# Kernel tuning notes

Hardware: AMD Instinct MI355X
Metric: run time of the kernel (lower is better)

Reference implementation:

```python
import jax, jax.numpy as jnp
import numpy as np

B, T, E, H = 4, 1024, 768, 12
DH = E // H
MAXP = 64  # rel_max_positions per relation type
SCALE = DH ** -0.5


def _sinusoid_embed(max_pos, dim):
    # fairseq-style sinusoid table with padding row 0 zeroed
    num = max_pos + 1
    half = dim // 2
    freq = np.exp(np.arange(half) * -(np.log(10000.0) / (half - 1)))
    ang = np.arange(num)[:, None] * freq[None, :]
    emb = np.concatenate([np.sin(ang), np.cos(ang)], axis=1)
    emb[0] = 0.0
    return jnp.asarray(emb, dtype=jnp.float32)


def _xavier(key, out_d, in_d, gain):
    bound = gain * np.sqrt(6.0 / (in_d + out_d))
    return jax.random.uniform(key, (out_d, in_d), jnp.float32, -bound, bound)


def setup_inputs() -> dict:
    key = jax.random.key(0)
    ks = jax.random.split(key, 16)
    g = 1.0 / np.sqrt(2.0)
    inp = {
        'x': jax.random.normal(ks[0], (B, T, E), jnp.float32),
        'rel_pos0': jax.random.randint(ks[1], (T, T), 0, MAXP + 1),
        'rel_pos1': jax.random.randint(ks[2], (T, T), 0, MAXP + 1),
        'rel_emb0': _sinusoid_embed(MAXP, E),
        'rel_emb1': _sinusoid_embed(MAXP, E),
    }
    names = ['Wq_r', 'Wk_r', 'Wv_r', 'Wq_s', 'Wk_s', 'Wv_s', 'Wk2', 'Wv2', 'Wrel0', 'Wrel1']
    for i, n in enumerate(names):
        inp[n] = _xavier(ks[3 + i], E, E, g)
        inp[n.replace('W', 'b', 1)] = jnp.zeros((E,), jnp.float32)
    inp['Wo'] = _xavier(ks[13], E, E, 1.0)
    inp['bo'] = jnp.zeros((E,), jnp.float32)
    return inp


def _lin(x, W, b):
    return x @ W.T + b


def _heads(x):
    return x.reshape(x.shape[0], x.shape[1], H, DH).transpose(0, 2, 1, 3)  # [B,H,T,DH]


def reference(x, rel_pos0, rel_pos1, rel_emb0, rel_emb1,
              Wq_r, bq_r, Wk_r, bk_r, Wv_r, bv_r,
              Wq_s, bq_s, Wk_s, bk_s, Wv_s, bv_s,
              Wk2, bk2, Wv2, bv2,
              Wrel0, brel0, Wrel1, brel1, Wo, bo):
    # --- sum branch: plain attention producing per-position summaries ---
    qs = _heads(_lin(x, Wq_s, bq_s)) * SCALE
    ks_ = _heads(_lin(x, Wk_s, bk_s))
    vs = _heads(_lin(x, Wv_s, bv_s))
    attn_s = jax.nn.softmax(jnp.einsum('bhqd,bhkd->bhqk', qs, ks_), axis=-1)
    sum_x = jnp.einsum('bhqk,bhkd->bhqd', attn_s, vs).transpose(0, 2, 1, 3).reshape(B, T, E)
    # summaries re-projected as extra keys/values for the reg branch
    k2 = _heads(_lin(sum_x, Wk2, bk2))
    v2 = _heads(_lin(sum_x, Wv2, bv2))
    # --- reg branch with per-relation-type RPE score biases ---
    q = _heads(_lin(x, Wq_r, bq_r)) * SCALE
    k = _heads(_lin(x, Wk_r, bk_r))
    v = _heads(_lin(x, Wv_r, bv_r))
    s_reg = jnp.einsum('bhqd,bhkd->bhqk', q, k)
    for rel_pos, rel_emb, Wr, br in ((rel_pos0, rel_emb0, Wrel0, brel0),
                                     (rel_pos1, rel_emb1, Wrel1, brel1)):
        table = _lin(rel_emb, Wr, br).reshape(-1, H, DH)       # [P,H,DH]
        ts = jnp.einsum('bhqd,phd->bhqp', q, table)            # [B,H,T,P]
        idx = jnp.broadcast_to(rel_pos[None, None], (B, H, T, T))
        s_reg = s_reg + jnp.take_along_axis(ts, idx, axis=3)   # RPE gather
    s_sum = jnp.einsum('bhqd,bhkd->bhqk', q, k2)
    attn = jax.nn.softmax(jnp.concatenate([s_reg, s_sum], axis=-1), axis=-1)  # [B,H,T,2T]
    kv = jnp.concatenate([v, v2], axis=2)                       # [B,H,2T,DH]
    out = jnp.einsum('bhqk,bhkd->bhqd', attn, kv).transpose(0, 2, 1, 3).reshape(B, T, E)
    return _lin(out, Wo, bo)
```

## Files before the change

kernel.cpp:

```cpp
#include <hip/hip_runtime.h>
#include <hip/hip_bf16.h>
#include <stdint.h>


#define DEV __device__ __forceinline__

using f32x4 = __attribute__((ext_vector_type(4))) float;
using s16x8 = __attribute__((ext_vector_type(8))) short;
using s16x4 = __attribute__((ext_vector_type(4))) short;
using i32x4 = __attribute__((ext_vector_type(4))) int;
using fvec4 = __attribute__((ext_vector_type(4))) float;
using u16 = unsigned short;

static constexpr int KD = 768;
static constexpr int PE = 4096 * 768;

DEV u16 f2bf(float f) {
  uint32_t u = __builtin_bit_cast(uint32_t, f);
  u += 0x7FFF + ((u >> 16) & 1);
  return (u16)(u >> 16);
}
DEV float bf2f(u16 h) { return __builtin_bit_cast(float, (uint32_t)h << 16); }

DEV void gload16(const void* g, void* l) {
  __builtin_amdgcn_global_load_lds((const __attribute__((address_space(1))) void*)g,
                                   (__attribute__((address_space(3))) void*)l, 16, 0, 0);
}
DEV f32x4 mfma16(s16x8 a, s16x8 b, f32x4 c) {
  return __builtin_amdgcn_mfma_f32_16x16x32_bf16(a, b, c, 0, 0, 0);
}

struct CastJobs {
  const float* src[14];
  u16* dst[14];
  int n[14];
};
__global__ __launch_bounds__(256) void cast_bf16_kernel(CastJobs J) {
  const int job = blockIdx.y;
  const int i = (blockIdx.x * 256 + threadIdx.x) * 8;
  if (i >= J.n[job]) return;
  const fvec4* s = (const fvec4*)(J.src[job] + i);
  fvec4 a = s[0], b = s[1];
  s16x8 o;
  o[0] = (short)f2bf(a[0]); o[1] = (short)f2bf(a[1]);
  o[2] = (short)f2bf(a[2]); o[3] = (short)f2bf(a[3]);
  o[4] = (short)f2bf(b[0]); o[5] = (short)f2bf(b[1]);
  o[6] = (short)f2bf(b[2]); o[7] = (short)f2bf(b[3]);
  *(s16x8*)(J.dst[job] + i) = o;
}

__global__ __launch_bounds__(256) void pack_rp_kernel(const int* rp0, const int* rp1, u16* outp) {
  const int i = (blockIdx.x * 256 + threadIdx.x) * 8;
  i32x4 a0 = *(const i32x4*)(rp0 + i), a1 = *(const i32x4*)(rp0 + i + 4);
  i32x4 b0 = *(const i32x4*)(rp1 + i), b1 = *(const i32x4*)(rp1 + i + 4);
  s16x8 o;
  o[0] = (short)(a0[0] | (b0[0] << 8));
  o[1] = (short)(a0[1] | (b0[1] << 8));
  o[2] = (short)(a0[2] | (b0[2] << 8));
  o[3] = (short)(a0[3] | (b0[3] << 8));
  o[4] = (short)(a1[0] | (b1[0] << 8));
  o[5] = (short)(a1[1] | (b1[1] << 8));
  o[6] = (short)(a1[2] | (b1[2] << 8));
  o[7] = (short)(a1[3] | (b1[3] << 8));
  *(s16x8*)(outp + i) = o;
}

struct GemmP {
  const u16* A;
  const u16* Bw;
  const float* bias[6];
  u16* out_bf;
  float* out_f;
  int epi;
};

__global__ __launch_bounds__(256) void gemm_bt(GemmP p) {
  __shared__ __align__(16) u16 As[128 * 64];
  __shared__ __align__(16) u16 Bs[128 * 64];
  const int tid = threadIdx.x;
  const int m0 = blockIdx.x * 128, n0 = blockIdx.y * 128;
  const u16* Ag = p.A + (size_t)m0 * KD;
  const u16* Bg = p.Bw + (size_t)n0 * KD;
  const int lane = tid & 63, wid = tid >> 6;
  const int wm = (wid >> 1) * 64, wn = (wid & 1) * 64;
  const int lhi = lane >> 4, llo = lane & 15;

  uint ldso[4], srco[4];
#pragma unroll
  for (int j = 0; j < 4; ++j) {
    uint o = tid * 16 + j * 4096;
    uint row = o >> 7, kc = (o >> 4) & 7;
    ldso[j] = o;
    srco[j] = row * KD + ((kc ^ (row & 7)) << 3);
  }

  f32x4 acc[4][4] = {};

  for (int kt = 0; kt < 12; ++kt) {
    const int k0 = kt * 64;
#pragma unroll
    for (int j = 0; j < 4; ++j) gload16(Ag + srco[j] + k0, (char*)As + ldso[j]);
#pragma unroll
    for (int j = 0; j < 4; ++j) gload16(Bg + srco[j] + k0, (char*)Bs + ldso[j]);
    __syncthreads();
#pragma unroll
    for (int kf = 0; kf < 2; ++kf) {
      s16x8 av[4], bv[4];
#pragma unroll
      for (int mf = 0; mf < 4; ++mf) {
        int r = wm + mf * 16 + llo;
        av[mf] = *(const s16x8*)&As[r * 64 + ((((kf << 2) | lhi) ^ (r & 7)) << 3)];
      }
#pragma unroll
      for (int nf = 0; nf < 4; ++nf) {
        int r = wn + nf * 16 + llo;
        bv[nf] = *(const s16x8*)&Bs[r * 64 + ((((kf << 2) | lhi) ^ (r & 7)) << 3)];
      }
#pragma unroll
      for (int mf = 0; mf < 4; ++mf)
#pragma unroll
        for (int nf = 0; nf < 4; ++nf)
          acc[mf][nf] = mfma16(av[mf], bv[nf], acc[mf][nf]);
    }
    __syncthreads();
  }

  const int epi = p.epi;
#pragma unroll
  for (int nf = 0; nf < 4; ++nf) {
    const int n = n0 + wn + nf * 16 + llo;
    int proj = 0, n1 = n, hh, dd;
    float bias, scale = 1.0f;
    if (epi <= 1) {
      proj = n / 768; n1 = n - proj * 768;
      hh = n1 >> 6; dd = n1 & 63;
      bias = p.bias[proj][n1];
      if (epi == 0 && (proj == 0 || proj == 3)) scale = 0.125f;
    } else {
      hh = n >> 6; dd = n & 63;
      bias = p.bias[0][n];
    }
#pragma unroll
    for (int mf = 0; mf < 4; ++mf) {
      f32x4 c = acc[mf][nf];
      const int mb = m0 + wm + mf * 16 + lhi * 4;
      if (epi == 3) {
#pragma unroll
        for (int r = 0; r < 4; ++r)
          p.out_f[(size_t)(mb + r) * 768 + n] = c[r] + bias;
      } else if (epi == 2) {
#pragma unroll
        for (int r = 0; r < 4; ++r) {
          int m = mb + r;
          if (m < 80) p.out_bf[((size_t)hh * 80 + m) * 64 + dd] = f2bf(c[r] + bias);
        }
      } else {
        const bool vlay = (epi == 0) ? (proj == 2 || proj == 5) : (proj == 1);
        if (vlay) {
          const int b = mb >> 10, t = mb & 1023;
          const int bh = b * 12 + hh;
          s16x4 o4;
          o4[0] = (short)f2bf((c[0] + bias) * scale);
          o4[1] = (short)f2bf((c[1] + bias) * scale);
          o4[2] = (short)f2bf((c[2] + bias) * scale);
          o4[3] = (short)f2bf((c[3] + bias) * scale);
          *(s16x4*)&p.out_bf[(size_t)proj * PE + ((size_t)(bh * 64 + dd)) * 1024 + t] = o4;
        } else {
#pragma unroll
          for (int r = 0; r < 4; ++r) {
            int m = mb + r;
            int b = m >> 10, t = m & 1023;
            int bh = b * 12 + hh;
            p.out_bf[(size_t)proj * PE + ((size_t)(bh * 1024 + t)) * 64 + dd] =
                f2bf((c[r] + bias) * scale);
          }
        }
      }
    }
  }
}

__global__ __launch_bounds__(256) void sum_attn_kernel(const u16* Qs, const u16* Ks,
                                                       const u16* Vst, u16* sum_x) {
  __shared__ __align__(16) u16 kbuf[64 * 64];
  __shared__ __align__(16) u16 vbuf[64 * 64];
  __shared__ __align__(16) u16 pbuf[4][16 * 72];
  const int tid = threadIdx.x, lane = tid & 63, w = tid >> 6;
  const int lhi = lane >> 4, llo = lane & 15;
  const int qt = blockIdx.x, bh = blockIdx.y;
  const int qbase = qt * 64 + w * 16;

  const u16* Qg = Qs + ((size_t)bh * 1024 + qbase + llo) * 64;
  s16x8 aq0 = *(const s16x8*)(Qg + lhi * 8);
  s16x8 aq1 = *(const s16x8*)(Qg + 32 + lhi * 8);

  f32x4 accO[4] = {};
  float mrun[4], lrun[4];
#pragma unroll
  for (int r = 0; r < 4; ++r) { mrun[r] = -1e30f; lrun[r] = 0.f; }

  uint so[2], srow[2], sswz[2];
#pragma unroll
  for (int j = 0; j < 2; ++j) {
    uint o = tid * 16 + j * 4096;
    so[j] = o; srow[j] = o >> 7;
    sswz[j] = (((o >> 4) & 7) ^ (srow[j] & 7)) << 3;
  }
  const u16* Kg = Ks + (size_t)bh * 65536;
  const u16* Vg = Vst + (size_t)bh * 65536;

  for (int kt = 0; kt < 16; ++kt) {
#pragma unroll
    for (int j = 0; j < 2; ++j) {
      gload16(Kg + (size_t)kt * 4096 + srow[j] * 64 + sswz[j], (char*)kbuf + so[j]);
      gload16(Vg + (size_t)srow[j] * 1024 + kt * 64 + sswz[j], (char*)vbuf + so[j]);
    }
    __syncthreads();

    f32x4 s[4];
#pragma unroll
    for (int kc4 = 0; kc4 < 4; ++kc4) {
      f32x4 c = {};
#pragma unroll
      for (int kf = 0; kf < 2; ++kf) {
        int kr = kc4 * 16 + llo;
        s16x8 bk = *(const s16x8*)&kbuf[kr * 64 + ((((kf << 2) | lhi) ^ (kr & 7)) << 3)];
        c = mfma16(kf ? aq1 : aq0, bk, c);
      }
      s[kc4] = c;
    }

    float pmax[4], corr[4], lpart[4];
#pragma unroll
    for (int r = 0; r < 4; ++r)
      pmax[r] = fmaxf(fmaxf(s[0][r], s[1][r]), fmaxf(s[2][r], s[3][r]));
#pragma unroll
    for (int msk = 1; msk < 16; msk <<= 1)
#pragma unroll
      for (int r = 0; r < 4; ++r)
        pmax[r] = fmaxf(pmax[r], __shfl_xor(pmax[r], msk, 64));
#pragma unroll
    for (int r = 0; r < 4; ++r) {
      float mn = fmaxf(mrun[r], pmax[r]);
      corr[r] = __expf(mrun[r] - mn);
      mrun[r] = mn; lpart[r] = 0.f;
    }
#pragma unroll
    for (int kc4 = 0; kc4 < 4; ++kc4)
#pragma unroll
      for (int r = 0; r < 4; ++r) {
        float pv = __expf(s[kc4][r] - mrun[r]);
        lpart[r] += pv;
        pbuf[w][(lhi * 4 + r) * 72 + kc4 * 16 + llo] = f2bf(pv);
      }
#pragma unroll
    for (int msk = 1; msk < 16; msk <<= 1)
#pragma unroll
      for (int r = 0; r < 4; ++r)
        lpart[r] += __shfl_xor(lpart[r], msk, 64);
#pragma unroll
    for (int r = 0; r < 4; ++r) lrun[r] = lrun[r] * corr[r] + lpart[r];
#pragma unroll
    for (int dc = 0; dc < 4; ++dc)
#pragma unroll
      for (int r = 0; r < 4; ++r) accO[dc][r] *= corr[r];

    asm volatile("s_waitcnt lgkmcnt(0)" ::: "memory");
    __builtin_amdgcn_sched_barrier(0);

#pragma unroll
    for (int kf = 0; kf < 2; ++kf) {
      s16x8 ap = *(const s16x8*)&pbuf[w][llo * 72 + kf * 32 + lhi * 8];
#pragma unroll
      for (int dc = 0; dc < 4; ++dc) {
        int dr = dc * 16 + llo;
        s16x8 bv = *(const s16x8*)&vbuf[dr * 64 + ((((kf << 2) | lhi) ^ (dr & 7)) << 3)];
        accO[dc] = mfma16(ap, bv, accO[dc]);
      }
    }
    __syncthreads();
  }

  const int b = bh / 12, hh = bh - b * 12;
#pragma unroll
  for (int dc = 0; dc < 4; ++dc)
#pragma unroll
    for (int r = 0; r < 4; ++r) {
      int q = qbase + lhi * 4 + r;
      float o = accO[dc][r] / lrun[r];
      sum_x[((size_t)b * 1024 + q) * 768 + hh * 64 + dc * 16 + llo] = f2bf(o);
    }
}

__global__ __launch_bounds__(256) void reg_attn_kernel(
    const u16* Qr, const u16* Kr, const u16* Vrt,
    const u16* K2, const u16* V2t,
    const u16* tab0, const u16* tab1,
    const u16* rpk, u16* attn_out) {
  __shared__ __align__(16) u16 kbuf[64 * 64];
  __shared__ __align__(16) u16 vbuf[64 * 64];
  __shared__ __align__(16) u16 tsb[2][64 * 80];
  __shared__ __align__(16) u16 pbuf[4][16 * 72];
  const int tid = threadIdx.x, lane = tid & 63, w = tid >> 6;
  const int lhi = lane >> 4, llo = lane & 15;
  const int qt = blockIdx.x, bh = blockIdx.y;
  const int b = bh / 12, hh = bh - b * 12;
  const int qbase = qt * 64 + w * 16;

  const u16* Qg = Qr + ((size_t)bh * 1024 + qbase + llo) * 64;
  s16x8 aq0 = *(const s16x8*)(Qg + lhi * 8);
  s16x8 aq1 = *(const s16x8*)(Qg + 32 + lhi * 8);

#pragma unroll
  for (int tt = 0; tt < 2; ++tt) {
    const u16* tb = tt ? tab1 : tab0;
#pragma unroll
    for (int pf = 0; pf < 5; ++pf) {
      f32x4 c = {};
#pragma unroll
      for (int kf = 0; kf < 2; ++kf) {
        s16x8 bt = *(const s16x8*)(tb + ((size_t)hh * 80 + pf * 16 + llo) * 64 + kf * 32 + lhi * 8);
        c = mfma16(kf ? aq1 : aq0, bt, c);
      }
#pragma unroll
      for (int r = 0; r < 4; ++r)
        tsb[tt][(w * 16 + lhi * 4 + r) * 80 + pf * 16 + llo] = f2bf(c[r]);
    }
  }
  __syncthreads();

  f32x4 accO[4] = {};
  float mrun[4], lrun[4];
#pragma unroll
  for (int r = 0; r < 4; ++r) { mrun[r] = -1e30f; lrun[r] = 0.f; }

  uint so[2], srow[2], sswz[2];
#pragma unroll
  for (int j = 0; j < 2; ++j) {
    uint o = tid * 16 + j * 4096;
    so[j] = o; srow[j] = o >> 7;
    sswz[j] = (((o >> 4) & 7) ^ (srow[j] & 7)) << 3;
  }
  const u16* KgA = Kr + (size_t)bh * 65536;
  const u16* KgB = K2 + (size_t)bh * 65536;
  const u16* VgA = Vrt + (size_t)bh * 65536;
  const u16* VgB = V2t + (size_t)bh * 65536;

  for (int kt = 0; kt < 32; ++kt) {
    const bool ph1 = kt < 16;
    const int kk = ph1 ? kt : kt - 16;
    const u16* Kg = ph1 ? KgA : KgB;
    const u16* Vg = ph1 ? VgA : VgB;
#pragma unroll
    for (int j = 0; j < 2; ++j) {
      gload16(Kg + (size_t)kk * 4096 + srow[j] * 64 + sswz[j], (char*)kbuf + so[j]);
      gload16(Vg + (size_t)srow[j] * 1024 + kk * 64 + sswz[j], (char*)vbuf + so[j]);
    }
    __syncthreads();

    f32x4 s[4];
#pragma unroll
    for (int kc4 = 0; kc4 < 4; ++kc4) {
      f32x4 c = {};
#pragma unroll
      for (int kf = 0; kf < 2; ++kf) {
        int kr = kc4 * 16 + llo;
        s16x8 bk = *(const s16x8*)&kbuf[kr * 64 + ((((kf << 2) | lhi) ^ (kr & 7)) << 3)];
        c = mfma16(kf ? aq1 : aq0, bk, c);
      }
      s[kc4] = c;
    }

    if (ph1) {
      u16 pp[16];
#pragma unroll
      for (int kc4 = 0; kc4 < 4; ++kc4)
#pragma unroll
        for (int r = 0; r < 4; ++r)
          pp[kc4 * 4 + r] =
              rpk[(size_t)(qbase + lhi * 4 + r) * 1024 + kt * 64 + kc4 * 16 + llo];
#pragma unroll
      for (int kc4 = 0; kc4 < 4; ++kc4)
#pragma unroll
        for (int r = 0; r < 4; ++r) {
          u16 v = pp[kc4 * 4 + r];
          int ql = w * 16 + lhi * 4 + r;
          s[kc4][r] += bf2f(tsb[0][ql * 80 + (v & 255)]) + bf2f(tsb[1][ql * 80 + (v >> 8)]);
        }
    }

    float pmax[4], corr[4], lpart[4];
#pragma unroll
    for (int r = 0; r < 4; ++r)
      pmax[r] = fmaxf(fmaxf(s[0][r], s[1][r]), fmaxf(s[2][r], s[3][r]));
#pragma unroll
    for (int msk = 1; msk < 16; msk <<= 1)
#pragma unroll
      for (int r = 0; r < 4; ++r)
        pmax[r] = fmaxf(pmax[r], __shfl_xor(pmax[r], msk, 64));
#pragma unroll
    for (int r = 0; r < 4; ++r) {
      float mn = fmaxf(mrun[r], pmax[r]);
      corr[r] = __expf(mrun[r] - mn);
      mrun[r] = mn; lpart[r] = 0.f;
    }
#pragma unroll
    for (int kc4 = 0; kc4 < 4; ++kc4)
#pragma unroll
      for (int r = 0; r < 4; ++r) {
        float pv = __expf(s[kc4][r] - mrun[r]);
        lpart[r] += pv;
        pbuf[w][(lhi * 4 + r) * 72 + kc4 * 16 + llo] = f2bf(pv);
      }
#pragma unroll
    for (int msk = 1; msk < 16; msk <<= 1)
#pragma unroll
      for (int r = 0; r < 4; ++r)
        lpart[r] += __shfl_xor(lpart[r], msk, 64);
#pragma unroll
    for (int r = 0; r < 4; ++r) lrun[r] = lrun[r] * corr[r] + lpart[r];
#pragma unroll
    for (int dc = 0; dc < 4; ++dc)
#pragma unroll
      for (int r = 0; r < 4; ++r) accO[dc][r] *= corr[r];

    asm volatile("s_waitcnt lgkmcnt(0)" ::: "memory");
    __builtin_amdgcn_sched_barrier(0);

#pragma unroll
    for (int kf = 0; kf < 2; ++kf) {
      s16x8 ap = *(const s16x8*)&pbuf[w][llo * 72 + kf * 32 + lhi * 8];
#pragma unroll
      for (int dc = 0; dc < 4; ++dc) {
        int dr = dc * 16 + llo;
        s16x8 bv = *(const s16x8*)&vbuf[dr * 64 + ((((kf << 2) | lhi) ^ (dr & 7)) << 3)];
        accO[dc] = mfma16(ap, bv, accO[dc]);
      }
    }
    __syncthreads();
  }

#pragma unroll
  for (int dc = 0; dc < 4; ++dc)
#pragma unroll
    for (int r = 0; r < 4; ++r) {
      int q = qbase + lhi * 4 + r;
      float o = accO[dc][r] / lrun[r];
      attn_out[((size_t)b * 1024 + q) * 768 + hh * 64 + dc * 16 + llo] = f2bf(o);
    }
}

extern "C" void kernel_launch(void* const* d_in, const int* in_sizes, int n_in,
                              void* d_out, int out_size, void* d_ws, size_t ws_size,
                              hipStream_t stream) {
  (void)in_sizes; (void)n_in; (void)out_size; (void)ws_size;
  const float* x     = (const float*)d_in[0];
  const int*   rp0   = (const int*)d_in[1];
  const int*   rp1   = (const int*)d_in[2];
  const float* re0   = (const float*)d_in[3];
  const float* re1   = (const float*)d_in[4];
  const float* Wq_r  = (const float*)d_in[5];  const float* bq_r = (const float*)d_in[6];
  const float* Wk_r  = (const float*)d_in[7];  const float* bk_r = (const float*)d_in[8];
  const float* Wv_r  = (const float*)d_in[9];  const float* bv_r = (const float*)d_in[10];
  const float* Wq_s  = (const float*)d_in[11]; const float* bq_s = (const float*)d_in[12];
  const float* Wk_s  = (const float*)d_in[13]; const float* bk_s = (const float*)d_in[14];
  const float* Wv_s  = (const float*)d_in[15]; const float* bv_s = (const float*)d_in[16];
  const float* Wk2   = (const float*)d_in[17]; const float* bk2  = (const float*)d_in[18];
  const float* Wv2   = (const float*)d_in[19]; const float* bv2  = (const float*)d_in[20];
  const float* Wrel0 = (const float*)d_in[21]; const float* brel0 = (const float*)d_in[22];
  const float* Wrel1 = (const float*)d_in[23]; const float* brel1 = (const float*)d_in[24];
  const float* Wo    = (const float*)d_in[25]; const float* bo   = (const float*)d_in[26];
  float* out = (float*)d_out;

  char* wp = (char*)d_ws;
  auto carve = [&](size_t bytes) {
    char* r = wp;
    wp += (bytes + 255) & ~(size_t)255;
    return r;
  };
  u16* xb     = (u16*)carve((size_t)PE * 2);
  u16* Wcat1  = (u16*)carve((size_t)4608 * 768 * 2);
  u16* Wcat2  = (u16*)carve((size_t)1536 * 768 * 2);
  u16* Wrel0b = (u16*)carve((size_t)768 * 768 * 2);
  u16* Wrel1b = (u16*)carve((size_t)768 * 768 * 2);
  u16* Wob    = (u16*)carve((size_t)768 * 768 * 2);
  u16* relA0  = (u16*)carve((size_t)128 * 768 * 2);
  u16* relA1  = (u16*)carve((size_t)128 * 768 * 2);
  u16* qkv    = (u16*)carve((size_t)6 * PE * 2);
  u16* k2v2   = (u16*)carve((size_t)2 * PE * 2);
  u16* tb0    = (u16*)carve((size_t)12 * 80 * 64 * 2);
  u16* tb1    = (u16*)carve((size_t)12 * 80 * 64 * 2);
  u16* rpk    = (u16*)carve((size_t)1024 * 1024 * 2);
  u16* sumx   = (u16*)carve((size_t)PE * 2);
  u16* aout   = (u16*)carve((size_t)PE * 2);

  const int wn_ = 768 * 768;
  CastJobs J;
  const float* srcs[14] = {x, Wq_r, Wk_r, Wv_r, Wq_s, Wk_s, Wv_s, Wk2, Wv2, Wrel0, Wrel1, Wo, re0, re1};
  u16* dsts[14] = {xb, Wcat1, Wcat1 + wn_, Wcat1 + 2 * wn_, Wcat1 + 3 * wn_, Wcat1 + 4 * wn_,
                   Wcat1 + 5 * wn_, Wcat2, Wcat2 + wn_, Wrel0b, Wrel1b, Wob, relA0, relA1};
  int ns[14] = {PE, wn_, wn_, wn_, wn_, wn_, wn_, wn_, wn_, wn_, wn_, wn_, 65 * 768, 65 * 768};
  for (int i = 0; i < 14; ++i) { J.src[i] = srcs[i]; J.dst[i] = dsts[i]; J.n[i] = ns[i]; }
  cast_bf16_kernel<<<dim3(1536, 14), 256, 0, stream>>>(J);

  pack_rp_kernel<<<dim3(512), 256, 0, stream>>>(rp0, rp1, rpk);

  GemmP g1{};
  g1.A = xb; g1.Bw = Wcat1;
  g1.bias[0] = bq_r; g1.bias[1] = bk_r; g1.bias[2] = bv_r;
  g1.bias[3] = bq_s; g1.bias[4] = bk_s; g1.bias[5] = bv_s;
  g1.out_bf = qkv; g1.epi = 0;
  gemm_bt<<<dim3(32, 36), 256, 0, stream>>>(g1);

  GemmP gt0{}; gt0.A = relA0; gt0.Bw = Wrel0b; gt0.bias[0] = brel0; gt0.out_bf = tb0; gt0.epi = 2;
  gemm_bt<<<dim3(1, 6), 256, 0, stream>>>(gt0);
  GemmP gt1{}; gt1.A = relA1; gt1.Bw = Wrel1b; gt1.bias[0] = brel1; gt1.out_bf = tb1; gt1.epi = 2;
  gemm_bt<<<dim3(1, 6), 256, 0, stream>>>(gt1);

  sum_attn_kernel<<<dim3(16, 48), 256, 0, stream>>>(qkv + (size_t)3 * PE, qkv + (size_t)4 * PE,
                                                    qkv + (size_t)5 * PE, sumx);

  GemmP g2{};
  g2.A = sumx; g2.Bw = Wcat2; g2.bias[0] = bk2; g2.bias[1] = bv2;
  g2.out_bf = k2v2; g2.epi = 1;
  gemm_bt<<<dim3(32, 12), 256, 0, stream>>>(g2);

  reg_attn_kernel<<<dim3(16, 48), 256, 0, stream>>>(qkv, qkv + (size_t)PE, qkv + (size_t)2 * PE,
                                                    k2v2, k2v2 + (size_t)PE, tb0, tb1, rpk, aout);

  GemmP gf{};
  gf.A = aout; gf.Bw = Wob; gf.bias[0] = bo; gf.out_f = out; gf.epi = 3;
  gemm_bt<<<dim3(32, 6), 256, 0, stream>>>(gf);
}
```

Before: 434.9 us.

## Lazy softmax rescale, deferred row-sum reduction, XCD-aware block remap in attention kernels

Both attention kernels now skip the cross-lane max reduction and accumulator rescale when no row max grows by more than 8 over the running max (wave-uniform check). Row sums stay as per-lane partials and are reduced once after the loop. Blocks are launched on a 1D grid and remapped so the 8 chunks of 96 consecutive (head, q-tile) work items each land on one XCD, improving L2 reuse of K/V. MFMA sections run under raised wave priority. The reg kernel splits its loop into two specialised phases and issues the RPE index loads before the barrier. The lazy max adds a small risk of bf16 precision loss when exp values reach up to e^8.

```diff
diff --git a/kernel.cpp b/kernel.cpp
--- a/kernel.cpp
+++ b/kernel.cpp
@@ -187,7 +187,9 @@
   __shared__ __align__(16) u16 pbuf[4][16 * 72];
   const int tid = threadIdx.x, lane = tid & 63, w = tid >> 6;
   const int lhi = lane >> 4, llo = lane & 15;
-  const int qt = blockIdx.x, bh = blockIdx.y;
+  const int bid = blockIdx.x;
+  const int vid = (bid & 7) * 96 + (bid >> 3);
+  const int qt = vid & 15, bh = vid >> 4;
   const int qbase = qt * 64 + w * 16;
 
   const u16* Qg = Qs + ((size_t)bh * 1024 + qbase + llo) * 64;
@@ -218,6 +220,7 @@
     __syncthreads();
 
     f32x4 s[4];
+    __builtin_amdgcn_s_setprio(1);
 #pragma unroll
     for (int kc4 = 0; kc4 < 4; ++kc4) {
       f32x4 c = {};
@@ -229,45 +232,47 @@
       }
       s[kc4] = c;
     }
-
-    float pmax[4], corr[4], lpart[4];
+    __builtin_amdgcn_s_setprio(0);
+
+    float smx[4];
 #pragma unroll
     for (int r = 0; r < 4; ++r)
-      pmax[r] = fmaxf(fmaxf(s[0][r], s[1][r]), fmaxf(s[2][r], s[3][r]));
-#pragma unroll
-    for (int msk = 1; msk < 16; msk <<= 1)
-#pragma unroll
-      for (int r = 0; r < 4; ++r)
-        pmax[r] = fmaxf(pmax[r], __shfl_xor(pmax[r], msk, 64));
+      smx[r] = fmaxf(fmaxf(s[0][r], s[1][r]), fmaxf(s[2][r], s[3][r]));
+    int ok = 1;
+#pragma unroll
+    for (int r = 0; r < 4; ++r) ok &= (smx[r] <= mrun[r] + 8.0f);
+    if (!__all(ok)) {
+#pragma unroll
+      for (int msk = 1; msk < 16; msk <<= 1)
+#pragma unroll
+        for (int r = 0; r < 4; ++r)
+          smx[r] = fmaxf(smx[r], __shfl_xor(smx[r], msk, 64));
+#pragma unroll
+      for (int r = 0; r < 4; ++r) {
+        float mn = fmaxf(mrun[r], smx[r]);
+        float corr = __expf(mrun[r] - mn);
+        mrun[r] = mn;
+        lrun[r] *= corr;
+#pragma unroll
+        for (int dc = 0; dc < 4; ++dc) accO[dc][r] *= corr;
+      }
+    }
 #pragma unroll
     for (int r = 0; r < 4; ++r) {
-      float mn = fmaxf(mrun[r], pmax[r]);
-      corr[r] = __expf(mrun[r] - mn);
-      mrun[r] = mn; lpart[r] = 0.f;
-    }
-#pragma unroll
-    for (int kc4 = 0; kc4 < 4; ++kc4)
-#pragma unroll
-      for (int r = 0; r < 4; ++r) {
+      float ls = 0.f;
+#pragma unroll
+      for (int kc4 = 0; kc4 < 4; ++kc4) {
         float pv = __expf(s[kc4][r] - mrun[r]);
-        lpart[r] += pv;
+        ls += pv;
         pbuf[w][(lhi * 4 + r) * 72 + kc4 * 16 + llo] = f2bf(pv);
       }
-#pragma unroll
-    for (int msk = 1; msk < 16; msk <<= 1)
-#pragma unroll
-      for (int r = 0; r < 4; ++r)
-        lpart[r] += __shfl_xor(lpart[r], msk, 64);
-#pragma unroll
-    for (int r = 0; r < 4; ++r) lrun[r] = lrun[r] * corr[r] + lpart[r];
-#pragma unroll
-    for (int dc = 0; dc < 4; ++dc)
-#pragma unroll
-      for (int r = 0; r < 4; ++r) accO[dc][r] *= corr[r];
+      lrun[r] += ls;
+    }
 
     asm volatile("s_waitcnt lgkmcnt(0)" ::: "memory");
     __builtin_amdgcn_sched_barrier(0);
 
+    __builtin_amdgcn_s_setprio(1);
 #pragma unroll
     for (int kf = 0; kf < 2; ++kf) {
       s16x8 ap = *(const s16x8*)&pbuf[w][llo * 72 + kf * 32 + lhi * 8];
@@ -278,8 +283,14 @@
         accO[dc] = mfma16(ap, bv, accO[dc]);
       }
     }
+    __builtin_amdgcn_s_setprio(0);
     __syncthreads();
   }
+
+#pragma unroll
+  for (int msk = 1; msk < 16; msk <<= 1)
+#pragma unroll
+    for (int r = 0; r < 4; ++r) lrun[r] += __shfl_xor(lrun[r], msk, 64);
 
   const int b = bh / 12, hh = bh - b * 12;
 #pragma unroll
@@ -303,7 +314,9 @@
   __shared__ __align__(16) u16 pbuf[4][16 * 72];
   const int tid = threadIdx.x, lane = tid & 63, w = tid >> 6;
   const int lhi = lane >> 4, llo = lane & 15;
-  const int qt = blockIdx.x, bh = blockIdx.y;
+  const int bid = blockIdx.x;
+  const int vid = (bid & 7) * 96 + (bid >> 3);
+  const int qt = vid & 15, bh = vid >> 4;
   const int b = bh / 12, hh = bh - b * 12;
   const int qbase = qt * 64 + w * 16;
 
@@ -333,6 +346,10 @@
   float mrun[4], lrun[4];
 #pragma unroll
   for (int r = 0; r < 4; ++r) { mrun[r] = -1e30f; lrun[r] = 0.f; }
+
+  int tbase[4];
+#pragma unroll
+  for (int r = 0; r < 4; ++r) tbase[r] = (w * 16 + lhi * 4 + r) * 80;
 
   uint so[2], srow[2], sswz[2];
 #pragma unroll
@@ -346,19 +363,25 @@
   const u16* VgA = Vrt + (size_t)bh * 65536;
   const u16* VgB = V2t + (size_t)bh * 65536;
 
-  for (int kt = 0; kt < 32; ++kt) {
-    const bool ph1 = kt < 16;
-    const int kk = ph1 ? kt : kt - 16;
-    const u16* Kg = ph1 ? KgA : KgB;
-    const u16* Vg = ph1 ? VgA : VgB;
+  auto tile = [&](const u16* Kg, const u16* Vg, int kk, bool gather) {
 #pragma unroll
     for (int j = 0; j < 2; ++j) {
       gload16(Kg + (size_t)kk * 4096 + srow[j] * 64 + sswz[j], (char*)kbuf + so[j]);
       gload16(Vg + (size_t)srow[j] * 1024 + kk * 64 + sswz[j], (char*)vbuf + so[j]);
     }
+    u16 pp[16];
+    if (gather) {
+#pragma unroll
+      for (int kc4 = 0; kc4 < 4; ++kc4)
+#pragma unroll
+        for (int r = 0; r < 4; ++r)
+          pp[kc4 * 4 + r] =
+              rpk[(size_t)(qbase + lhi * 4 + r) * 1024 + kk * 64 + kc4 * 16 + llo];
+    }
     __syncthreads();
 
     f32x4 s[4];
+    __builtin_amdgcn_s_setprio(1);
 #pragma unroll
     for (int kc4 = 0; kc4 < 4; ++kc4) {
       f32x4 c = {};
@@ -370,63 +393,57 @@
       }
       s[kc4] = c;
     }
-
-    if (ph1) {
-      u16 pp[16];
-#pragma unroll
-      for (int kc4 = 0; kc4 < 4; ++kc4)
-#pragma unroll
-        for (int r = 0; r < 4; ++r)
-          pp[kc4 * 4 + r] =
-              rpk[(size_t)(qbase + lhi * 4 + r) * 1024 + kt * 64 + kc4 * 16 + llo];
+    __builtin_amdgcn_s_setprio(0);
+
+    if (gather) {
 #pragma unroll
       for (int kc4 = 0; kc4 < 4; ++kc4)
 #pragma unroll
         for (int r = 0; r < 4; ++r) {
           u16 v = pp[kc4 * 4 + r];
-          int ql = w * 16 + lhi * 4 + r;
-          s[kc4][r] += bf2f(tsb[0][ql * 80 + (v & 255)]) + bf2f(tsb[1][ql * 80 + (v >> 8)]);
+          s[kc4][r] += bf2f(tsb[0][tbase[r] + (v & 255)]) + bf2f(tsb[1][tbase[r] + (v >> 8)]);
         }
     }
 
-    float pmax[4], corr[4], lpart[4];
+    float smx[4];
 #pragma unroll
     for (int r = 0; r < 4; ++r)
-      pmax[r] = fmaxf(fmaxf(s[0][r], s[1][r]), fmaxf(s[2][r], s[3][r]));
-#pragma unroll
-    for (int msk = 1; msk < 16; msk <<= 1)
-#pragma unroll
-      for (int r = 0; r < 4; ++r)
-        pmax[r] = fmaxf(pmax[r], __shfl_xor(pmax[r], msk, 64));
+      smx[r] = fmaxf(fmaxf(s[0][r], s[1][r]), fmaxf(s[2][r], s[3][r]));
+    int ok = 1;
+#pragma unroll
+    for (int r = 0; r < 4; ++r) ok &= (smx[r] <= mrun[r] + 8.0f);
+    if (!__all(ok)) {
+#pragma unroll
+      for (int msk = 1; msk < 16; msk <<= 1)
+#pragma unroll
+        for (int r = 0; r < 4; ++r)
+          smx[r] = fmaxf(smx[r], __shfl_xor(smx[r], msk, 64));
+#pragma unroll
+      for (int r = 0; r < 4; ++r) {
+        float mn = fmaxf(mrun[r], smx[r]);
+        float corr = __expf(mrun[r] - mn);
+        mrun[r] = mn;
+        lrun[r] *= corr;
+#pragma unroll
+        for (int dc = 0; dc < 4; ++dc) accO[dc][r] *= corr;
+      }
+    }
 #pragma unroll
     for (int r = 0; r < 4; ++r) {
-      float mn = fmaxf(mrun[r], pmax[r]);
-      corr[r] = __expf(mrun[r] - mn);
-      mrun[r] = mn; lpart[r] = 0.f;
-    }
-#pragma unroll
-    for (int kc4 = 0; kc4 < 4; ++kc4)
-#pragma unroll
-      for (int r = 0; r < 4; ++r) {
+      float ls = 0.f;
+#pragma unroll
+      for (int kc4 = 0; kc4 < 4; ++kc4) {
         float pv = __expf(s[kc4][r] - mrun[r]);
-        lpart[r] += pv;
+        ls += pv;
         pbuf[w][(lhi * 4 + r) * 72 + kc4 * 16 + llo] = f2bf(pv);
       }
-#pragma unroll
-    for (int msk = 1; msk < 16; msk <<= 1)
-#pragma unroll
-      for (int r = 0; r < 4; ++r)
-        lpart[r] += __shfl_xor(lpart[r], msk, 64);
-#pragma unroll
-    for (int r = 0; r < 4; ++r) lrun[r] = lrun[r] * corr[r] + lpart[r];
-#pragma unroll
-    for (int dc = 0; dc < 4; ++dc)
-#pragma unroll
-      for (int r = 0; r < 4; ++r) accO[dc][r] *= corr[r];
+      lrun[r] += ls;
+    }
 
     asm volatile("s_waitcnt lgkmcnt(0)" ::: "memory");
     __builtin_amdgcn_sched_barrier(0);
 
+    __builtin_amdgcn_s_setprio(1);
 #pragma unroll
     for (int kf = 0; kf < 2; ++kf) {
       s16x8 ap = *(const s16x8*)&pbuf[w][llo * 72 + kf * 32 + lhi * 8];
@@ -437,8 +454,17 @@
         accO[dc] = mfma16(ap, bv, accO[dc]);
       }
     }
+    __builtin_amdgcn_s_setprio(0);
     __syncthreads();
-  }
+  };
+
+  for (int kt = 0; kt < 16; ++kt) tile(KgA, VgA, kt, true);
+  for (int kt = 0; kt < 16; ++kt) tile(KgB, VgB, kt, false);
+
+#pragma unroll
+  for (int msk = 1; msk < 16; msk <<= 1)
+#pragma unroll
+    for (int r = 0; r < 4; ++r) lrun[r] += __shfl_xor(lrun[r], msk, 64);
 
 #pragma unroll
   for (int dc = 0; dc < 4; ++dc)
@@ -517,16 +543,16 @@
   GemmP gt1{}; gt1.A = relA1; gt1.Bw = Wrel1b; gt1.bias[0] = brel1; gt1.out_bf = tb1; gt1.epi = 2;
   gemm_bt<<<dim3(1, 6), 256, 0, stream>>>(gt1);
 
-  sum_attn_kernel<<<dim3(16, 48), 256, 0, stream>>>(qkv + (size_t)3 * PE, qkv + (size_t)4 * PE,
-                                                    qkv + (size_t)5 * PE, sumx);
+  sum_attn_kernel<<<dim3(768), 256, 0, stream>>>(qkv + (size_t)3 * PE, qkv + (size_t)4 * PE,
+                                                 qkv + (size_t)5 * PE, sumx);
 
   GemmP g2{};
   g2.A = sumx; g2.Bw = Wcat2; g2.bias[0] = bk2; g2.bias[1] = bv2;
   g2.out_bf = k2v2; g2.epi = 1;
   gemm_bt<<<dim3(32, 12), 256, 0, stream>>>(g2);
 
-  reg_attn_kernel<<<dim3(16, 48), 256, 0, stream>>>(qkv, qkv + (size_t)PE, qkv + (size_t)2 * PE,
-                                                    k2v2, k2v2 + (size_t)PE, tb0, tb1, rpk, aout);
+  reg_attn_kernel<<<dim3(768), 256, 0, stream>>>(qkv, qkv + (size_t)PE, qkv + (size_t)2 * PE,
+                                                 k2v2, k2v2 + (size_t)PE, tb0, tb1, rpk, aout);
 
   GemmP gf{};
   gf.A = aout; gf.Bw = Wob; gf.bias[0] = bo; gf.out_f = out; gf.epi = 3;
```

After: 386.5 us. 11.1% less time.
